# Performance work log

Hardware: AMD Instinct MI355X
Metric: run time of the kernel (lower is better)

The kernel has to match this reference:

```python
import jax, jax.numpy as jnp
import numpy as np


def setup_inputs() -> dict:
    key = jax.random.key(0)
    k1, k2, k3 = jax.random.split(key, 3)
    B, T1, T2, D = 16, 1024, 1024, 256
    x = jax.random.normal(k1, (B, T1, D), dtype=jnp.float32)
    y = jax.random.normal(k2, (B, T2, D), dtype=jnp.float32)
    WS = jax.random.normal(k3, (3 * D,), dtype=jnp.float32) * 0.05
    return {"x": x, "y": y, "WS": WS}


def reference(x, y, WS):
    # BiDAF trilinear similarity. Original computes
    #   S[b,i,j] = sum_k concat([x_i, 1, x_i])_k * concat([1, y_j, y_j])_k * WS_k
    # which decomposes exactly into:
    #   S = x @ w1 (broadcast over j) + y @ w2 (broadcast over i) + (x * w3) @ y^T
    D = x.shape[-1]
    w1, w2, w3 = WS[:D], WS[D:2 * D], WS[2 * D:]
    term_x = jnp.einsum('bid,d->bi', x, w1)            # [B, T1]
    term_y = jnp.einsum('bjd,d->bj', y, w2)            # [B, T2]
    term_xy = jnp.einsum('bid,bjd->bij', x * w3, y)    # [B, T1, T2]
    return term_xy + term_x[:, :, None] + term_y[:, None, :]
```

## Files before the change

### kernel.cpp

```cpp
#include <hip/hip_runtime.h>

#define DK 256
#define TT 1024
#define NB 16

typedef __attribute__((ext_vector_type(8))) short bf16x8;
typedef __attribute__((ext_vector_type(4))) float f32x4;

__device__ __forceinline__ unsigned short f2bf(float f) {
    unsigned int u = __float_as_uint(f);
    unsigned int r = 0x7fffu + ((u >> 16) & 1u);
    return (unsigned short)((u + r) >> 16);
}

__global__ __launch_bounds__(256) void prep_kernel(
    const float* __restrict__ x, const float* __restrict__ y,
    const float* __restrict__ WS,
    unsigned short* __restrict__ xw, unsigned short* __restrict__ yb,
    float* __restrict__ tx, float* __restrict__ ty)
{
    const int wid  = threadIdx.x >> 6;
    const int lane = threadIdx.x & 63;
    const int row  = blockIdx.x * 4 + wid;
    const bool is_x = row < NB * TT;
    const int r = is_x ? row : row - NB * TT;

    const float4 wmul = is_x ? ((const float4*)(WS + 2 * DK))[lane]
                             : make_float4(1.f, 1.f, 1.f, 1.f);
    const float4 wdot = is_x ? ((const float4*)WS)[lane]
                             : ((const float4*)(WS + DK))[lane];

    const float4 v = ((const float4*)((is_x ? x : y) + (size_t)r * DK))[lane];

    float partial = v.x * wdot.x + v.y * wdot.y + v.z * wdot.z + v.w * wdot.w;

    ushort4 o;
    o.x = f2bf(v.x * wmul.x);
    o.y = f2bf(v.y * wmul.y);
    o.z = f2bf(v.z * wmul.z);
    o.w = f2bf(v.w * wmul.w);
    ((ushort4*)((is_x ? xw : yb) + (size_t)r * DK))[lane] = o;

    #pragma unroll
    for (int off = 32; off > 0; off >>= 1)
        partial += __shfl_down(partial, off);
    if (lane == 0) (is_x ? tx : ty)[r] = partial;
}

__device__ __forceinline__ void gl_lds16(const unsigned short* g,
                                         unsigned short* l)
{
    __builtin_amdgcn_global_load_lds(
        (const __attribute__((address_space(1))) void*)g,
        (__attribute__((address_space(3))) void*)l,
        16, 0, 0);
}

__global__ __launch_bounds__(256) void gemm_kernel(
    const unsigned short* __restrict__ xw, const unsigned short* __restrict__ yb,
    const float* __restrict__ tx, const float* __restrict__ ty,
    float* __restrict__ out)
{
    __shared__ unsigned short As[128 * 64];
    __shared__ unsigned short Bs[128 * 64];
    __shared__ float txs[128];
    __shared__ float tys[128];

    const int tid  = threadIdx.x;
    const int w    = tid >> 6;
    const int lane = tid & 63;
    const int wi   = w >> 1;
    const int wj   = w & 1;
    const int batch = blockIdx.z;
    const int it = blockIdx.y;
    const int jt = blockIdx.x;

    const unsigned short* gA = xw + ((size_t)batch * TT + it * 128) * DK;
    const unsigned short* gB = yb + ((size_t)batch * TT + jt * 128) * DK;

    if (tid < 128) txs[tid] = tx[batch * TT + it * 128 + tid];
    else           tys[tid - 128] = ty[batch * TT + jt * 128 + tid - 128];

    f32x4 acc[4][4];
    #pragma unroll
    for (int i = 0; i < 4; ++i)
        #pragma unroll
        for (int j = 0; j < 4; ++j)
            acc[i][j] = (f32x4){0.f, 0.f, 0.f, 0.f};

    const int mfr  = lane & 15;
    const int quad = lane >> 4;

    #pragma unroll
    for (int kt = 0; kt < 4; ++kt) {
        #pragma unroll
        for (int q = 0; q < 4; ++q) {
            const int m0   = w * 32 + q * 8;
            const int m    = m0 + (lane >> 3);
            const int slot = lane & 7;
            const int kc   = slot ^ (m & 7);
            gl_lds16(gA + (size_t)m * DK + kt * 64 + kc * 8, As + m0 * 64);
            gl_lds16(gB + (size_t)m * DK + kt * 64 + kc * 8, Bs + m0 * 64);
        }
        __syncthreads();

        #pragma unroll
        for (int ks = 0; ks < 2; ++ks) {
            const int kc = ks * 4 + quad;
            bf16x8 av[4], bv[4];
            #pragma unroll
            for (int mi = 0; mi < 4; ++mi) {
                const int m = wi * 64 + mi * 16 + mfr;
                av[mi] = *(const bf16x8*)(As + m * 64 + (kc ^ (m & 7)) * 8);
                const int n = wj * 64 + mi * 16 + mfr;
                bv[mi] = *(const bf16x8*)(Bs + n * 64 + (kc ^ (n & 7)) * 8);
            }
            #pragma unroll
            for (int mi = 0; mi < 4; ++mi)
                #pragma unroll
                for (int ni = 0; ni < 4; ++ni)
                    acc[mi][ni] = __builtin_amdgcn_mfma_f32_16x16x32_bf16(
                        av[mi], bv[ni], acc[mi][ni], 0, 0, 0);
        }
        __syncthreads();
    }

    float* outB = out + ((size_t)batch << 20) + (size_t)(it * 128) * TT + jt * 128;
    #pragma unroll
    for (int mi = 0; mi < 4; ++mi) {
        #pragma unroll
        for (int r = 0; r < 4; ++r) {
            const int row = wi * 64 + mi * 16 + quad * 4 + r;
            const float trow = txs[row];
            #pragma unroll
            for (int ni = 0; ni < 4; ++ni) {
                const int col = wj * 64 + ni * 16 + mfr;
                outB[(size_t)row * TT + col] = acc[mi][ni][r] + trow + tys[col];
            }
        }
    }
}

__global__ __launch_bounds__(256) void naive_kernel(
    const float* __restrict__ x, const float* __restrict__ y,
    const float* __restrict__ WS, float* __restrict__ out)
{
    size_t idx = (size_t)blockIdx.x * 256 + threadIdx.x;
    if (idx >= (size_t)NB * TT * TT) return;
    const int b = (int)(idx >> 20);
    const int i = (int)((idx >> 10) & (TT - 1));
    const int j = (int)(idx & (TT - 1));
    const float* xp = x + ((size_t)b * TT + i) * DK;
    const float* yp = y + ((size_t)b * TT + j) * DK;
    float s = 0.f, sx = 0.f, sy = 0.f;
    for (int d = 0; d < DK; ++d) {
        const float xv = xp[d], yv = yp[d];
        s  += xv * WS[2 * DK + d] * yv;
        sx += xv * WS[d];
        sy += yv * WS[DK + d];
    }
    out[idx] = s + sx + sy;
}

extern "C" void kernel_launch(void* const* d_in, const int* in_sizes, int n_in,
                              void* d_out, int out_size, void* d_ws, size_t ws_size,
                              hipStream_t stream)
{
    const float* x  = (const float*)d_in[0];
    const float* y  = (const float*)d_in[1];
    const float* WS = (const float*)d_in[2];
    float* out = (float*)d_out;

    const size_t n_xy = (size_t)NB * TT * DK;
    const size_t need = n_xy * 2 * sizeof(unsigned short)
                      + (size_t)NB * TT * 2 * sizeof(float);

    if (ws_size >= need) {
        unsigned short* xw = (unsigned short*)d_ws;
        unsigned short* yb = xw + n_xy;
        float* tx = (float*)(yb + n_xy);
        float* ty = tx + NB * TT;

        prep_kernel<<<dim3((2 * NB * TT) / 4), dim3(256), 0, stream>>>(
            x, y, WS, xw, yb, tx, ty);
        gemm_kernel<<<dim3(8, 8, NB), dim3(256), 0, stream>>>(
            xw, yb, tx, ty, out);
    } else {
        naive_kernel<<<dim3((NB * TT * TT + 255) / 256), dim3(256), 0, stream>>>(
            x, y, WS, out);
    }
}
```

Before: 112.3 us.

## Double-buffer LDS tiles in GEMM and read bias terms from global

Splits the A/B shared-memory tiles into two buffers so the next K-slice is prefetched with global_load_lds while MFMAs run on the current one. This leaves one barrier per K step instead of two. The tx/ty bias values are now read directly from global memory in the epilogue rather than staged in LDS. The cost is twice the LDS per block, which can lower how many blocks fit on each CU, and the pipeline has only four K iterations to hide latency over.

```diff
diff --git a/kernel.cpp b/kernel.cpp
--- a/kernel.cpp
+++ b/kernel.cpp
@@ -61,10 +61,8 @@
     const float* __restrict__ tx, const float* __restrict__ ty,
     float* __restrict__ out)
 {
-    __shared__ unsigned short As[128 * 64];
-    __shared__ unsigned short Bs[128 * 64];
-    __shared__ float txs[128];
-    __shared__ float tys[128];
+    __shared__ unsigned short As[2][128 * 64];
+    __shared__ unsigned short Bs[2][128 * 64];
 
     const int tid  = threadIdx.x;
     const int w    = tid >> 6;
@@ -78,8 +76,9 @@
     const unsigned short* gA = xw + ((size_t)batch * TT + it * 128) * DK;
     const unsigned short* gB = yb + ((size_t)batch * TT + jt * 128) * DK;
 
-    if (tid < 128) txs[tid] = tx[batch * TT + it * 128 + tid];
-    else           tys[tid - 128] = ty[batch * TT + jt * 128 + tid - 128];
+    const int sm0_base = w * 32;
+    const int srow     = lane >> 3;
+    const int sslot    = lane & 7;
 
     f32x4 acc[4][4];
     #pragma unroll
@@ -92,18 +91,34 @@
     const int quad = lane >> 4;
 
     #pragma unroll
+    for (int q = 0; q < 4; ++q) {
+        const int m0 = sm0_base + q * 8;
+        const int m  = m0 + srow;
+        const int kc = sslot ^ (m & 7);
+        gl_lds16(gA + (size_t)m * DK + kc * 8, &As[0][m0 * 64]);
+        gl_lds16(gB + (size_t)m * DK + kc * 8, &Bs[0][m0 * 64]);
+    }
+
+    #pragma unroll
     for (int kt = 0; kt < 4; ++kt) {
-        #pragma unroll
-        for (int q = 0; q < 4; ++q) {
-            const int m0   = w * 32 + q * 8;
-            const int m    = m0 + (lane >> 3);
-            const int slot = lane & 7;
-            const int kc   = slot ^ (m & 7);
-            gl_lds16(gA + (size_t)m * DK + kt * 64 + kc * 8, As + m0 * 64);
-            gl_lds16(gB + (size_t)m * DK + kt * 64 + kc * 8, Bs + m0 * 64);
+        __syncthreads();
+
+        if (kt < 3) {
+            const int buf = (kt + 1) & 1;
+            #pragma unroll
+            for (int q = 0; q < 4; ++q) {
+                const int m0 = sm0_base + q * 8;
+                const int m  = m0 + srow;
+                const int kc = sslot ^ (m & 7);
+                gl_lds16(gA + (size_t)m * DK + (kt + 1) * 64 + kc * 8,
+                         &As[buf][m0 * 64]);
+                gl_lds16(gB + (size_t)m * DK + (kt + 1) * 64 + kc * 8,
+                         &Bs[buf][m0 * 64]);
+            }
         }
-        __syncthreads();
-
+
+        const unsigned short* Ab = As[kt & 1];
+        const unsigned short* Bb = Bs[kt & 1];
         #pragma unroll
         for (int ks = 0; ks < 2; ++ks) {
             const int kc = ks * 4 + quad;
@@ -111,9 +126,9 @@
             #pragma unroll
             for (int mi = 0; mi < 4; ++mi) {
                 const int m = wi * 64 + mi * 16 + mfr;
-                av[mi] = *(const bf16x8*)(As + m * 64 + (kc ^ (m & 7)) * 8);
+                av[mi] = *(const bf16x8*)(Ab + m * 64 + (kc ^ (m & 7)) * 8);
                 const int n = wj * 64 + mi * 16 + mfr;
-                bv[mi] = *(const bf16x8*)(Bs + n * 64 + (kc ^ (n & 7)) * 8);
+                bv[mi] = *(const bf16x8*)(Bb + n * 64 + (kc ^ (n & 7)) * 8);
             }
             #pragma unroll
             for (int mi = 0; mi < 4; ++mi)
@@ -122,20 +137,26 @@
                     acc[mi][ni] = __builtin_amdgcn_mfma_f32_16x16x32_bf16(
                         av[mi], bv[ni], acc[mi][ni], 0, 0, 0);
         }
-        __syncthreads();
-    }
+    }
+
+    const float* txp = tx + batch * TT + it * 128;
+    const float* typ = ty + batch * TT + jt * 128;
+    float tyv[4];
+    #pragma unroll
+    for (int ni = 0; ni < 4; ++ni)
+        tyv[ni] = typ[wj * 64 + ni * 16 + mfr];
 
     float* outB = out + ((size_t)batch << 20) + (size_t)(it * 128) * TT + jt * 128;
     #pragma unroll
     for (int mi = 0; mi < 4; ++mi) {
         #pragma unroll
         for (int r = 0; r < 4; ++r) {
-            const int row = wi * 64 + mi * 16 + quad * 4 + r;
-            const float trow = txs[row];
+            const int row  = wi * 64 + mi * 16 + quad * 4 + r;
+            const float trow = txp[row];
             #pragma unroll
             for (int ni = 0; ni < 4; ++ni) {
                 const int col = wj * 64 + ni * 16 + mfr;
-                outB[(size_t)row * TT + col] = acc[mi][ni][r] + trow + tys[col];
+                outB[(size_t)row * TT + col] = acc[mi][ni][r] + trow + tyv[ni];
             }
         }
     }
```

New measurement: 113.3 us. About the same (+1.0%).

## Stage full-K B tile in LDS and stream A fragments directly from global

Applied to the files above, without the earlier changes.

The GEMM kernel now loads the entire 128x256 bf16 B tile into LDS once, with an XOR swizzle, and syncs only once. A fragments are read straight from global memory into registers. Each wave computes a 64x128 output block over a 256x128 block tile, and the grid is halved in y. This removes the per-k-step double barrier and LDS staging of A, and doubles per-wave reuse of B. In exchange it adds uncoalesced global loads for A on the critical path, uses 64 KB of LDS per block, and raises register pressure, which may limit occupancy despite the launch bound of 2.

```diff
diff --git a/kernel.cpp b/kernel.cpp
--- a/kernel.cpp
+++ b/kernel.cpp
@@ -56,87 +56,80 @@
         16, 0, 0);
 }
 
-__global__ __launch_bounds__(256) void gemm_kernel(
+__global__ __launch_bounds__(256, 2) void gemm_kernel(
     const unsigned short* __restrict__ xw, const unsigned short* __restrict__ yb,
     const float* __restrict__ tx, const float* __restrict__ ty,
     float* __restrict__ out)
 {
-    __shared__ unsigned short As[128 * 64];
-    __shared__ unsigned short Bs[128 * 64];
-    __shared__ float txs[128];
-    __shared__ float tys[128];
+    __shared__ unsigned short Bs[128 * DK];
 
     const int tid  = threadIdx.x;
     const int w    = tid >> 6;
     const int lane = tid & 63;
-    const int wi   = w >> 1;
-    const int wj   = w & 1;
-    const int batch = blockIdx.z;
-    const int it = blockIdx.y;
     const int jt = blockIdx.x;
+    const int is = blockIdx.y;
+    const int b  = blockIdx.z;
 
-    const unsigned short* gA = xw + ((size_t)batch * TT + it * 128) * DK;
-    const unsigned short* gB = yb + ((size_t)batch * TT + jt * 128) * DK;
+    const unsigned short* gB = yb + ((size_t)b * TT + jt * 128) * DK;
 
-    if (tid < 128) txs[tid] = tx[batch * TT + it * 128 + tid];
-    else           tys[tid - 128] = ty[batch * TT + jt * 128 + tid - 128];
-
-    f32x4 acc[4][4];
     #pragma unroll
-    for (int i = 0; i < 4; ++i)
-        #pragma unroll
-        for (int j = 0; j < 4; ++j)
-            acc[i][j] = (f32x4){0.f, 0.f, 0.f, 0.f};
+    for (int q = 0; q < 16; ++q) {
+        const int g = w * 16 + q;
+        const int j = g * 2 + (lane >> 5);
+        const int s = lane & 31;
+        const int c = s ^ (j & 7);
+        gl_lds16(gB + j * DK + c * 8, Bs + g * 512);
+    }
+    __syncthreads();
 
     const int mfr  = lane & 15;
     const int quad = lane >> 4;
+    const int i0   = is * 256 + w * 64;
+    const unsigned short* gA = xw + ((size_t)b * TT + i0) * DK;
+
+    f32x4 acc[4][8];
+    #pragma unroll
+    for (int it = 0; it < 4; ++it)
+        #pragma unroll
+        for (int n = 0; n < 8; ++n)
+            acc[it][n] = (f32x4){0.f, 0.f, 0.f, 0.f};
 
     #pragma unroll
-    for (int kt = 0; kt < 4; ++kt) {
+    for (int ks = 0; ks < 8; ++ks) {
+        bf16x8 av[4];
         #pragma unroll
-        for (int q = 0; q < 4; ++q) {
-            const int m0   = w * 32 + q * 8;
-            const int m    = m0 + (lane >> 3);
-            const int slot = lane & 7;
-            const int kc   = slot ^ (m & 7);
-            gl_lds16(gA + (size_t)m * DK + kt * 64 + kc * 8, As + m0 * 64);
-            gl_lds16(gB + (size_t)m * DK + kt * 64 + kc * 8, Bs + m0 * 64);
+        for (int it = 0; it < 4; ++it)
+            av[it] = *(const bf16x8*)(gA + (size_t)(it * 16 + mfr) * DK
+                                      + ks * 32 + quad * 8);
+        #pragma unroll
+        for (int n = 0; n < 8; ++n) {
+            const int j    = n * 16 + mfr;
+            const int slot = (ks * 4 + quad) ^ (j & 7);
+            const bf16x8 bv = *(const bf16x8*)(Bs + j * DK + slot * 8);
+            #pragma unroll
+            for (int it = 0; it < 4; ++it)
+                acc[it][n] = __builtin_amdgcn_mfma_f32_16x16x32_bf16(
+                    av[it], bv, acc[it][n], 0, 0, 0);
         }
-        __syncthreads();
-
-        #pragma unroll
-        for (int ks = 0; ks < 2; ++ks) {
-            const int kc = ks * 4 + quad;
-            bf16x8 av[4], bv[4];
-            #pragma unroll
-            for (int mi = 0; mi < 4; ++mi) {
-                const int m = wi * 64 + mi * 16 + mfr;
-                av[mi] = *(const bf16x8*)(As + m * 64 + (kc ^ (m & 7)) * 8);
-                const int n = wj * 64 + mi * 16 + mfr;
-                bv[mi] = *(const bf16x8*)(Bs + n * 64 + (kc ^ (n & 7)) * 8);
-            }
-            #pragma unroll
-            for (int mi = 0; mi < 4; ++mi)
-                #pragma unroll
-                for (int ni = 0; ni < 4; ++ni)
-                    acc[mi][ni] = __builtin_amdgcn_mfma_f32_16x16x32_bf16(
-                        av[mi], bv[ni], acc[mi][ni], 0, 0, 0);
-        }
-        __syncthreads();
     }
 
-    float* outB = out + ((size_t)batch << 20) + (size_t)(it * 128) * TT + jt * 128;
+    const float* txp = tx + b * TT + i0;
+    const float* typ = ty + b * TT + jt * 128;
+    float tyv[8];
     #pragma unroll
-    for (int mi = 0; mi < 4; ++mi) {
+    for (int n = 0; n < 8; ++n)
+        tyv[n] = typ[n * 16 + mfr];
+
+    float* outB = out + ((size_t)b << 20) + (size_t)i0 * TT + jt * 128;
+    #pragma unroll
+    for (int it = 0; it < 4; ++it) {
         #pragma unroll
         for (int r = 0; r < 4; ++r) {
-            const int row = wi * 64 + mi * 16 + quad * 4 + r;
-            const float trow = txs[row];
+            const int row  = it * 16 + quad * 4 + r;
+            const float trow = txp[row];
             #pragma unroll
-            for (int ni = 0; ni < 4; ++ni) {
-                const int col = wj * 64 + ni * 16 + mfr;
-                outB[(size_t)row * TT + col] = acc[mi][ni][r] + trow + tys[col];
-            }
+            for (int n = 0; n < 8; ++n)
+                outB[(size_t)row * TT + n * 16 + mfr] = acc[it][n][r] + trow + tyv[n];
         }
     }
 }
@@ -183,7 +176,7 @@
 
         prep_kernel<<<dim3((2 * NB * TT) / 4), dim3(256), 0, stream>>>(
             x, y, WS, xw, yb, tx, ty);
-        gemm_kernel<<<dim3(8, 8, NB), dim3(256), 0, stream>>>(
+        gemm_kernel<<<dim3(8, 4, NB), dim3(256), 0, stream>>>(
             xw, yb, tx, ty, out);
     } else {
         naive_kernel<<<dim3((NB * TT * TT + 255) / 256), dim3(256), 0, stream>>>(
```

Result: no change. 111.0 us (-1.1%).
